# Kernel tuning notes

Hardware: AMD Instinct MI355X
Metric: run time of the kernel (lower is better)

Reference implementation:

```python
import jax, jax.numpy as jnp
import numpy as np

B, N, M = 1024, 65536, 128


def setup_inputs() -> dict:
    key = jax.random.key(0)
    k1, k2, k3, k4 = jax.random.split(key, 4)
    address = jax.random.uniform(k1, (B, N), dtype=jnp.float32)
    erase = jax.random.uniform(k2, (B, M), dtype=jnp.float32)
    add = jax.random.normal(k3, (B, M), dtype=jnp.float32)
    content = jax.random.uniform(k4, (N, M), dtype=jnp.float32)
    return {"address": address, "erase": erase, "add": add, "content": content}


def reference(address, erase, add, content):
    # write: outer-product erase/add aggregated over batch -> [N, M]
    erase_v = jnp.einsum('bn,bm->nm', address, erase)
    add_v = jnp.einsum('bn,bm->nm', address, add)
    new_content = content * (1.0 - erase_v) + add_v
    # read-after-write: [B,N] @ [N,M] -> [B,M]
    read_content = jnp.einsum('bn,nm->bm', address, new_content)
    return read_content
```

## Files before the change

kernel.cpp:

```cpp
#include <hip/hip_runtime.h>
#include <hip/hip_bf16.h>
#include <stdint.h>

#define B_SZ 1024
#define N_SZ 65536
#define M_SZ 128

typedef short bf16x8 __attribute__((ext_vector_type(8)));
typedef short bf16x4 __attribute__((ext_vector_type(4)));
typedef float f32x4 __attribute__((ext_vector_type(4)));

__device__ __forceinline__ unsigned short f2bf(float f) {
    uint32_t u = __float_as_uint(f);
    uint32_t r = (u + 0x7FFFu + ((u >> 16) & 1u)) >> 16;
    return (unsigned short)r;
}

__global__ __launch_bounds__(256) void k_edt(const float* __restrict__ E,
                                             const float* __restrict__ D,
                                             unsigned short* __restrict__ EDt) {
    __shared__ float tile[32][33];
    int bx = blockIdx.x & 31;
    int cy = blockIdx.x >> 5;
    int b0 = bx * 32, c0 = cy * 32;
    const float* src = (c0 < M_SZ) ? E : D;
    int cs0 = c0 & (M_SZ - 1);
    int t = threadIdx.x;
    int i = t >> 3, j = (t & 7) * 4;
    const float* p = src + (size_t)(b0 + i) * M_SZ + cs0 + j;
    float4 v = *(const float4*)p;
    tile[i][j] = v.x; tile[i][j + 1] = v.y; tile[i][j + 2] = v.z; tile[i][j + 3] = v.w;
    __syncthreads();
    int c = t >> 3, b4 = (t & 7) * 4;
    unsigned short* q = EDt + (size_t)(c0 + c) * B_SZ + b0 + b4;
    ushort4 o;
    o.x = f2bf(tile[b4 + 0][c]); o.y = f2bf(tile[b4 + 1][c]);
    o.z = f2bf(tile[b4 + 2][c]); o.w = f2bf(tile[b4 + 3][c]);
    *(ushort4*)q = o;
}

#define AS_LD 132

__global__ __launch_bounds__(256, 2) void k_pass1(
    const float* __restrict__ A,
    const unsigned short* __restrict__ EDt,
    const float* __restrict__ C,
    unsigned short* __restrict__ NCt)
{
    __shared__ __align__(16) unsigned short As[2][32 * AS_LD];
    __shared__ __align__(16) unsigned short EDs[2][256 * 32];
    const int t = threadIdx.x;
    const int lane = t & 63;
    const int wv = t >> 6;
    const int wvn = wv >> 1, wvc = wv & 1;
    const int g = lane >> 4;
    const int m16 = lane & 15;
    const int n0 = blockIdx.x * 128;

    const int kb = t >> 3;
    const int cA = (t & 7) * 16;

    int cb[8];
#pragma unroll
    for (int fj = 0; fj < 4; ++fj) { cb[fj] = wvc * 4 + fj; cb[fj + 4] = 8 + wvc * 4 + fj; }

    f32x4 acc[4][8];
#pragma unroll
    for (int i = 0; i < 4; ++i)
#pragma unroll
        for (int j = 0; j < 8; ++j) acc[i][j] = (f32x4){0.f, 0.f, 0.f, 0.f};

#define ED_GLLDS(buf, bkv)                                                          \
    {                                                                               \
        _Pragma("unroll")                                                           \
        for (int i_ = 0; i_ < 4; ++i_) {                                            \
            int L_ = i_ * 256 + t;                                                  \
            int col_ = L_ >> 2;                                                     \
            int ss_ = (L_ & 3) ^ ((col_ >> 1) & 3);                                 \
            const unsigned short* gsrc_ = EDt + (size_t)col_ * B_SZ + (bkv) + ss_ * 8; \
            __builtin_amdgcn_global_load_lds(                                       \
                (const __attribute__((address_space(1))) uint32_t*)(const void*)gsrc_, \
                (__attribute__((address_space(3))) uint32_t*)(void*)&EDs[buf][(i_ * 256 + wv * 64) * 8], \
                16, 0, 0);                                                          \
        }                                                                           \
    }

#define A_LOAD(dst0, dst1, dst2, dst3, bkv)                                         \
    {                                                                               \
        const float* p_ = A + (size_t)((bkv) + kb) * N_SZ + n0 + cA;                \
        dst0 = ((const float4*)p_)[0]; dst1 = ((const float4*)p_)[1];               \
        dst2 = ((const float4*)p_)[2]; dst3 = ((const float4*)p_)[3];               \
    }

#define A_WRITE(buf, s0, s1, s2, s3)                                                \
    {                                                                               \
        ushort4* w_ = (ushort4*)&As[buf][kb * AS_LD + cA];                          \
        ushort4 o_;                                                                 \
        o_.x = f2bf(s0.x); o_.y = f2bf(s0.y); o_.z = f2bf(s0.z); o_.w = f2bf(s0.w); w_[0] = o_; \
        o_.x = f2bf(s1.x); o_.y = f2bf(s1.y); o_.z = f2bf(s1.z); o_.w = f2bf(s1.w); w_[1] = o_; \
        o_.x = f2bf(s2.x); o_.y = f2bf(s2.y); o_.z = f2bf(s2.z); o_.w = f2bf(s2.w); w_[2] = o_; \
        o_.x = f2bf(s3.x); o_.y = f2bf(s3.y); o_.z = f2bf(s3.z); o_.w = f2bf(s3.w); w_[3] = o_; \
    }

#define P1_COMPUTE(buf)                                                             \
    {                                                                               \
        bf16x8 af_[4];                                                              \
        _Pragma("unroll")                                                           \
        for (int fi = 0; fi < 4; ++fi) {                                            \
            int nl_ = wvn * 64 + fi * 16 + m16;                                     \
            _Pragma("unroll")                                                       \
            for (int j = 0; j < 8; ++j)                                             \
                af_[fi][j] = (short)As[buf][(g * 8 + j) * AS_LD + nl_];              \
        }                                                                           \
        bf16x8 bfr_[8];                                                             \
        _Pragma("unroll")                                                           \
        for (int fj = 0; fj < 8; ++fj) {                                            \
            int col_ = cb[fj] * 16 + m16;                                           \
            bfr_[fj] = *(const bf16x8*)&EDs[buf][col_ * 32 + ((g ^ ((col_ >> 1) & 3)) << 3)]; \
        }                                                                           \
        _Pragma("unroll")                                                           \
        for (int fj = 0; fj < 8; ++fj)                                              \
            _Pragma("unroll")                                                       \
            for (int fi = 0; fi < 4; ++fi)                                          \
                acc[fi][fj] = __builtin_amdgcn_mfma_f32_16x16x32_bf16(af_[fi], bfr_[fj], acc[fi][fj], 0, 0, 0); \
    }

    float4 ra0_0, ra0_1, ra0_2, ra0_3;
    float4 ra1_0, ra1_1, ra1_2, ra1_3;

    A_LOAD(ra0_0, ra0_1, ra0_2, ra0_3, 0)
    ED_GLLDS(0, 0)
    A_WRITE(0, ra0_0, ra0_1, ra0_2, ra0_3)
    A_LOAD(ra1_0, ra1_1, ra1_2, ra1_3, 32)
    __syncthreads();

    for (int c = 0; c < 32; c += 2) {
        if (c + 1 < 32) ED_GLLDS(1, (c + 1) * 32)
        if (c + 2 < 32) A_LOAD(ra0_0, ra0_1, ra0_2, ra0_3, (c + 2) * 32)
        P1_COMPUTE(0)
        if (c + 1 < 32) A_WRITE(1, ra1_0, ra1_1, ra1_2, ra1_3)
        __syncthreads();
        if (c + 1 < 32) {
            if (c + 2 < 32) ED_GLLDS(0, (c + 2) * 32)
            if (c + 3 < 32) A_LOAD(ra1_0, ra1_1, ra1_2, ra1_3, (c + 3) * 32)
            P1_COMPUTE(1)
            if (c + 2 < 32) A_WRITE(0, ra0_0, ra0_1, ra0_2, ra0_3)
            __syncthreads();
        }
    }

#pragma unroll
    for (int fi = 0; fi < 4; ++fi)
#pragma unroll
        for (int fj = 0; fj < 4; ++fj) {
            int n_base = n0 + wvn * 64 + fi * 16 + g * 4;
            int m = wvc * 64 + fj * 16 + m16;
            bf16x4 o;
#pragma unroll
            for (int r = 0; r < 4; ++r) {
                float w = acc[fi][fj][r];
                float v = acc[fi][fj + 4][r];
                float cc = C[(size_t)(n_base + r) * M_SZ + m];
                o[r] = (short)f2bf(cc * (1.0f - w) + v);
            }
            *(bf16x4*)&NCt[(size_t)m * N_SZ + n_base] = o;
        }
}

#define L2_LD 40

__global__ __launch_bounds__(256, 2) void k_pass2(
    const float* __restrict__ A,
    const unsigned short* __restrict__ NCt,
    float* __restrict__ part)
{
    __shared__ __align__(16) unsigned short As2[2][128 * L2_LD];
    __shared__ __align__(16) unsigned short NCs[2][128 * L2_LD];
    const int t = threadIdx.x;
    const int lane = t & 63;
    const int wv = t >> 6;
    const int wvb = wv >> 1, wvm = wv & 1;
    const int g = lane >> 4;
    const int m16 = lane & 15;
    const int b0 = (blockIdx.x & 7) * 128;
    const int ks = blockIdx.x >> 3;
    const int k0 = ks << 10;

    const int row = t >> 1, half = t & 1;

    f32x4 acc[4][4];
#pragma unroll
    for (int i = 0; i < 4; ++i)
#pragma unroll
        for (int j = 0; j < 4; ++j) acc[i][j] = (f32x4){0.f, 0.f, 0.f, 0.f};

    {
        const float* p = A + (size_t)(b0 + row) * N_SZ + k0 + half * 16;
        float4 a0 = ((const float4*)p)[0], a1 = ((const float4*)p)[1];
        float4 a2 = ((const float4*)p)[2], a3 = ((const float4*)p)[3];
        ushort4* w = (ushort4*)&As2[0][row * L2_LD + half * 16];
        ushort4 o;
        o.x = f2bf(a0.x); o.y = f2bf(a0.y); o.z = f2bf(a0.z); o.w = f2bf(a0.w); w[0] = o;
        o.x = f2bf(a1.x); o.y = f2bf(a1.y); o.z = f2bf(a1.z); o.w = f2bf(a1.w); w[1] = o;
        o.x = f2bf(a2.x); o.y = f2bf(a2.y); o.z = f2bf(a2.z); o.w = f2bf(a2.w); w[2] = o;
        o.x = f2bf(a3.x); o.y = f2bf(a3.y); o.z = f2bf(a3.z); o.w = f2bf(a3.w); w[3] = o;
        const uint4* pn = (const uint4*)(NCt + (size_t)row * N_SZ + k0 + half * 16);
        uint4 n0v = pn[0], n1v = pn[1];
        uint4* wn = (uint4*)&NCs[0][row * L2_LD + half * 16];
        wn[0] = n0v; wn[1] = n1v;
    }
    __syncthreads();

    int cur = 0;
    for (int kk = 0; kk < 1024; kk += 32) {
        const bool last = (kk + 32 >= 1024);
        const int nkk = last ? 0 : kk + 32;

        const float* p = A + (size_t)(b0 + row) * N_SZ + k0 + nkk + half * 16;
        float4 a0 = ((const float4*)p)[0], a1 = ((const float4*)p)[1];
        float4 a2 = ((const float4*)p)[2], a3 = ((const float4*)p)[3];
        const uint4* pn = (const uint4*)(NCt + (size_t)row * N_SZ + k0 + nkk + half * 16);
        uint4 n0v = pn[0], n1v = pn[1];

        bf16x8 af[4];
#pragma unroll
        for (int fi = 0; fi < 4; ++fi)
            af[fi] = *(const bf16x8*)&As2[cur][(wvb * 64 + fi * 16 + m16) * L2_LD + g * 8];
        bf16x8 bfr[4];
#pragma unroll
        for (int fj = 0; fj < 4; ++fj)
            bfr[fj] = *(const bf16x8*)&NCs[cur][(wvm * 64 + fj * 16 + m16) * L2_LD + g * 8];

#pragma unroll
        for (int fi = 0; fi < 4; ++fi)
#pragma unroll
            for (int fj = 0; fj < 4; ++fj)
                acc[fi][fj] = __builtin_amdgcn_mfma_f32_16x16x32_bf16(af[fi], bfr[fj], acc[fi][fj], 0, 0, 0);

        if (!last) {
            const int nxt = cur ^ 1;
            ushort4* w = (ushort4*)&As2[nxt][row * L2_LD + half * 16];
            ushort4 o;
            o.x = f2bf(a0.x); o.y = f2bf(a0.y); o.z = f2bf(a0.z); o.w = f2bf(a0.w); w[0] = o;
            o.x = f2bf(a1.x); o.y = f2bf(a1.y); o.z = f2bf(a1.z); o.w = f2bf(a1.w); w[1] = o;
            o.x = f2bf(a2.x); o.y = f2bf(a2.y); o.z = f2bf(a2.z); o.w = f2bf(a2.w); w[2] = o;
            o.x = f2bf(a3.x); o.y = f2bf(a3.y); o.z = f2bf(a3.z); o.w = f2bf(a3.w); w[3] = o;
            uint4* wn = (uint4*)&NCs[nxt][row * L2_LD + half * 16];
            wn[0] = n0v; wn[1] = n1v;
        }
        __syncthreads();
        cur ^= 1;
    }

    float* pp = part + (size_t)ks * (B_SZ * M_SZ);
#pragma unroll
    for (int fi = 0; fi < 4; ++fi)
#pragma unroll
        for (int fj = 0; fj < 4; ++fj)
#pragma unroll
            for (int r = 0; r < 4; ++r) {
                int b = b0 + wvb * 64 + fi * 16 + g * 4 + r;
                int m = wvm * 64 + fj * 16 + m16;
                pp[(size_t)b * M_SZ + m] = acc[fi][fj][r];
            }
}

__global__ __launch_bounds__(256) void k_reduce(const float* __restrict__ part,
                                                float* __restrict__ out) {
    const int idx4 = blockIdx.x * 256 + threadIdx.x;
    const float* p = part + (size_t)idx4 * 4;
    f32x4 s0 = {0.f,0.f,0.f,0.f}, s1 = s0, s2 = s0, s3 = s0;
#pragma unroll
    for (int s = 0; s < 64; s += 4) {
        f32x4 v0 = *(const f32x4*)(p + (size_t)(s + 0) * (B_SZ * M_SZ));
        f32x4 v1 = *(const f32x4*)(p + (size_t)(s + 1) * (B_SZ * M_SZ));
        f32x4 v2 = *(const f32x4*)(p + (size_t)(s + 2) * (B_SZ * M_SZ));
        f32x4 v3 = *(const f32x4*)(p + (size_t)(s + 3) * (B_SZ * M_SZ));
        s0 += v0; s1 += v1; s2 += v2; s3 += v3;
    }
    f32x4 r = (s0 + s1) + (s2 + s3);
    *(f32x4*)(out + (size_t)idx4 * 4) = r;
}

extern "C" void kernel_launch(void* const* d_in, const int* in_sizes, int n_in,
                              void* d_out, int out_size, void* d_ws, size_t ws_size,
                              hipStream_t stream) {
    const float* A  = (const float*)d_in[0];
    const float* E  = (const float*)d_in[1];
    const float* Dd = (const float*)d_in[2];
    const float* C  = (const float*)d_in[3];
    float* out = (float*)d_out;

    unsigned short* NCt = (unsigned short*)d_ws;
    unsigned short* EDt = (unsigned short*)((char*)d_ws + (size_t)M_SZ * N_SZ * 2);
    float* part = (float*)((char*)d_ws + (size_t)M_SZ * N_SZ * 2 + (size_t)256 * B_SZ * 2);

    k_edt   <<<256, 256, 0, stream>>>(E, Dd, EDt);
    k_pass1 <<<512, 256, 0, stream>>>(A, EDt, C, NCt);
    k_pass2 <<<512, 256, 0, stream>>>(A, NCt, part);
    k_reduce<<<128, 256, 0, stream>>>(part, out);
}
```

Baseline: 152.0 us.

## Load NCt tiles directly into LDS with swizzled layout and deeper A prefetch

In the pass-2 GEMM kernel, the bf16 new-content tiles are now copied from global memory straight into LDS with global_load_lds, skipping the register round trip. The LDS rows are unpadded and use an XOR swizzle to avoid bank conflicts. The loop is unrolled by two with two register sets for A, so A prefetch runs two stages ahead. The goal is to cut register pressure and VALU/LDS-store work, and to hide more global latency behind the MFMAs. In exchange, correctness now depends on the async LDS writes being visible once the existing barriers complete.

```diff
diff --git a/kernel.cpp b/kernel.cpp
--- a/kernel.cpp
+++ b/kernel.cpp
@@ -175,7 +175,7 @@
     float* __restrict__ part)
 {
     __shared__ __align__(16) unsigned short As2[2][128 * L2_LD];
-    __shared__ __align__(16) unsigned short NCs[2][128 * L2_LD];
+    __shared__ __align__(16) unsigned short NCs[2][128 * 32];
     const int t = threadIdx.x;
     const int lane = t & 63;
     const int wv = t >> 6;
@@ -194,62 +194,79 @@
 #pragma unroll
         for (int j = 0; j < 4; ++j) acc[i][j] = (f32x4){0.f, 0.f, 0.f, 0.f};
 
-    {
-        const float* p = A + (size_t)(b0 + row) * N_SZ + k0 + half * 16;
-        float4 a0 = ((const float4*)p)[0], a1 = ((const float4*)p)[1];
-        float4 a2 = ((const float4*)p)[2], a3 = ((const float4*)p)[3];
-        ushort4* w = (ushort4*)&As2[0][row * L2_LD + half * 16];
-        ushort4 o;
-        o.x = f2bf(a0.x); o.y = f2bf(a0.y); o.z = f2bf(a0.z); o.w = f2bf(a0.w); w[0] = o;
-        o.x = f2bf(a1.x); o.y = f2bf(a1.y); o.z = f2bf(a1.z); o.w = f2bf(a1.w); w[1] = o;
-        o.x = f2bf(a2.x); o.y = f2bf(a2.y); o.z = f2bf(a2.z); o.w = f2bf(a2.w); w[2] = o;
-        o.x = f2bf(a3.x); o.y = f2bf(a3.y); o.z = f2bf(a3.z); o.w = f2bf(a3.w); w[3] = o;
-        const uint4* pn = (const uint4*)(NCt + (size_t)row * N_SZ + k0 + half * 16);
-        uint4 n0v = pn[0], n1v = pn[1];
-        uint4* wn = (uint4*)&NCs[0][row * L2_LD + half * 16];
-        wn[0] = n0v; wn[1] = n1v;
-    }
+#define NC_GLLDS(buf, kkv)                                                          \
+    {                                                                               \
+        _Pragma("unroll")                                                           \
+        for (int i_ = 0; i_ < 2; ++i_) {                                            \
+            int L_ = i_ * 256 + t;                                                  \
+            int row_ = L_ >> 2;                                                     \
+            int ss_ = (L_ & 3) ^ ((row_ >> 1) & 3);                                 \
+            const unsigned short* gsrc_ = NCt + (size_t)row_ * N_SZ + k0 + (kkv) + ss_ * 8; \
+            __builtin_amdgcn_global_load_lds(                                       \
+                (const __attribute__((address_space(1))) uint32_t*)(const void*)gsrc_, \
+                (__attribute__((address_space(3))) uint32_t*)(void*)&NCs[buf][L_ * 8], \
+                16, 0, 0);                                                          \
+        }                                                                           \
+    }
+
+#define A2_LOAD(dst0, dst1, dst2, dst3, kkv)                                        \
+    {                                                                               \
+        const float* p_ = A + (size_t)(b0 + row) * N_SZ + k0 + (kkv) + half * 16;   \
+        dst0 = ((const float4*)p_)[0]; dst1 = ((const float4*)p_)[1];               \
+        dst2 = ((const float4*)p_)[2]; dst3 = ((const float4*)p_)[3];               \
+    }
+
+#define A2_WRITE(buf, s0, s1, s2, s3)                                               \
+    {                                                                               \
+        ushort4* w_ = (ushort4*)&As2[buf][row * L2_LD + half * 16];                 \
+        ushort4 o_;                                                                 \
+        o_.x = f2bf(s0.x); o_.y = f2bf(s0.y); o_.z = f2bf(s0.z); o_.w = f2bf(s0.w); w_[0] = o_; \
+        o_.x = f2bf(s1.x); o_.y = f2bf(s1.y); o_.z = f2bf(s1.z); o_.w = f2bf(s1.w); w_[1] = o_; \
+        o_.x = f2bf(s2.x); o_.y = f2bf(s2.y); o_.z = f2bf(s2.z); o_.w = f2bf(s2.w); w_[2] = o_; \
+        o_.x = f2bf(s3.x); o_.y = f2bf(s3.y); o_.z = f2bf(s3.z); o_.w = f2bf(s3.w); w_[3] = o_; \
+    }
+
+#define P2_COMPUTE(buf)                                                             \
+    {                                                                               \
+        bf16x8 af_[4];                                                              \
+        _Pragma("unroll")                                                           \
+        for (int fi = 0; fi < 4; ++fi)                                              \
+            af_[fi] = *(const bf16x8*)&As2[buf][(wvb * 64 + fi * 16 + m16) * L2_LD + g * 8]; \
+        bf16x8 bfr_[4];                                                             \
+        _Pragma("unroll")                                                           \
+        for (int fj = 0; fj < 4; ++fj) {                                            \
+            int row_ = wvm * 64 + fj * 16 + m16;                                    \
+            bfr_[fj] = *(const bf16x8*)&NCs[buf][row_ * 32 + ((g ^ ((row_ >> 1) & 3)) << 3)]; \
+        }                                                                           \
+        _Pragma("unroll")                                                           \
+        for (int fi = 0; fi < 4; ++fi)                                              \
+            _Pragma("unroll")                                                       \
+            for (int fj = 0; fj < 4; ++fj)                                          \
+                acc[fi][fj] = __builtin_amdgcn_mfma_f32_16x16x32_bf16(af_[fi], bfr_[fj], acc[fi][fj], 0, 0, 0); \
+    }
+
+    float4 rb0_0, rb0_1, rb0_2, rb0_3;
+    float4 rb1_0, rb1_1, rb1_2, rb1_3;
+
+    A2_LOAD(rb0_0, rb0_1, rb0_2, rb0_3, 0)
+    NC_GLLDS(0, 0)
+    A2_WRITE(0, rb0_0, rb0_1, rb0_2, rb0_3)
+    A2_LOAD(rb1_0, rb1_1, rb1_2, rb1_3, 32)
     __syncthreads();
 
-    int cur = 0;
-    for (int kk = 0; kk < 1024; kk += 32) {
-        const bool last = (kk + 32 >= 1024);
-        const int nkk = last ? 0 : kk + 32;
-
-        const float* p = A + (size_t)(b0 + row) * N_SZ + k0 + nkk + half * 16;
-        float4 a0 = ((const float4*)p)[0], a1 = ((const float4*)p)[1];
-        float4 a2 = ((const float4*)p)[2], a3 = ((const float4*)p)[3];
-        const uint4* pn = (const uint4*)(NCt + (size_t)row * N_SZ + k0 + nkk + half * 16);
-        uint4 n0v = pn[0], n1v = pn[1];
-
-        bf16x8 af[4];
-#pragma unroll
-        for (int fi = 0; fi < 4; ++fi)
-            af[fi] = *(const bf16x8*)&As2[cur][(wvb * 64 + fi * 16 + m16) * L2_LD + g * 8];
-        bf16x8 bfr[4];
-#pragma unroll
-        for (int fj = 0; fj < 4; ++fj)
-            bfr[fj] = *(const bf16x8*)&NCs[cur][(wvm * 64 + fj * 16 + m16) * L2_LD + g * 8];
-
-#pragma unroll
-        for (int fi = 0; fi < 4; ++fi)
-#pragma unroll
-            for (int fj = 0; fj < 4; ++fj)
-                acc[fi][fj] = __builtin_amdgcn_mfma_f32_16x16x32_bf16(af[fi], bfr[fj], acc[fi][fj], 0, 0, 0);
-
-        if (!last) {
-            const int nxt = cur ^ 1;
-            ushort4* w = (ushort4*)&As2[nxt][row * L2_LD + half * 16];
-            ushort4 o;
-            o.x = f2bf(a0.x); o.y = f2bf(a0.y); o.z = f2bf(a0.z); o.w = f2bf(a0.w); w[0] = o;
-            o.x = f2bf(a1.x); o.y = f2bf(a1.y); o.z = f2bf(a1.z); o.w = f2bf(a1.w); w[1] = o;
-            o.x = f2bf(a2.x); o.y = f2bf(a2.y); o.z = f2bf(a2.z); o.w = f2bf(a2.w); w[2] = o;
-            o.x = f2bf(a3.x); o.y = f2bf(a3.y); o.z = f2bf(a3.z); o.w = f2bf(a3.w); w[3] = o;
-            uint4* wn = (uint4*)&NCs[nxt][row * L2_LD + half * 16];
-            wn[0] = n0v; wn[1] = n1v;
+    for (int c = 0; c < 32; c += 2) {
+        if (c + 1 < 32) NC_GLLDS(1, (c + 1) * 32)
+        if (c + 2 < 32) A2_LOAD(rb0_0, rb0_1, rb0_2, rb0_3, (c + 2) * 32)
+        P2_COMPUTE(0)
+        if (c + 1 < 32) A2_WRITE(1, rb1_0, rb1_1, rb1_2, rb1_3)
+        __syncthreads();
+        if (c + 1 < 32) {
+            if (c + 2 < 32) NC_GLLDS(0, (c + 2) * 32)
+            if (c + 3 < 32) A2_LOAD(rb1_0, rb1_1, rb1_2, rb1_3, (c + 3) * 32)
+            P2_COMPUTE(1)
+            if (c + 2 < 32) A2_WRITE(0, rb0_0, rb0_1, rb0_2, rb0_3)
+            __syncthreads();
         }
-        __syncthreads();
-        cur ^= 1;
     }
 
     float* pp = part + (size_t)ks * (B_SZ * M_SZ);
```

Measured after the change: 151.4 us. Within noise of the previous version (-0.4%).
